# Kernel tuning notes

Hardware: AMD Instinct MI355X
Metric: run time of the kernel (lower is better)

Reference implementation:

```python
import jax, jax.numpy as jnp
import numpy as np

VOCAB = 1024
PRED_H = 320
ENC_H = 1024
JOINT_H = 640


def setup_inputs() -> dict:
    key = jax.random.key(0)
    k_f, k_g, k_w1, k_b1, k_w2, k_b2 = jax.random.split(key, 6)
    B, T, U = 8, 256, 65
    f = jax.random.normal(k_f, (B, T, ENC_H), dtype=jnp.float32)
    g = jax.random.normal(k_g, (B, U, PRED_H), dtype=jnp.float32)
    in_dim = PRED_H + ENC_H
    s1 = 1.0 / np.sqrt(in_dim)
    s2 = 1.0 / np.sqrt(JOINT_H)
    # W1 acts on cat([f, g], axis=-1): rows [0:ENC_H] hit f, rows [ENC_H:] hit g
    W1 = jax.random.uniform(k_w1, (in_dim, JOINT_H), minval=-s1, maxval=s1, dtype=jnp.float32)
    b1 = jax.random.uniform(k_b1, (JOINT_H,), minval=-s1, maxval=s1, dtype=jnp.float32)
    W2 = jax.random.uniform(k_w2, (JOINT_H, VOCAB), minval=-s2, maxval=s2, dtype=jnp.float32)
    b2 = jax.random.uniform(k_b2, (VOCAB,), minval=-s2, maxval=s2, dtype=jnp.float32)
    return {"f": f, "g": g, "W1": W1, "b1": b1, "W2": W2, "b2": b2}


def reference(f, g, W1, b1, W2, b2):
    # Linear(cat(f_expand, g_expand)) == f @ W1[:ENC_H] + g @ W1[ENC_H:] + b1,
    # broadcast-added over (T, U). Same math as the torch module (dropout p=0 / eval).
    W1f = W1[:ENC_H]          # (ENC_H, JOINT_H)
    W1g = W1[ENC_H:]          # (PRED_H, JOINT_H)
    hf = jnp.einsum("bth,hj->btj", f, W1f)            # (B, T, J)
    hg = jnp.einsum("buh,hj->buj", g, W1g)            # (B, U, J)
    h = jax.nn.relu(hf[:, :, None, :] + hg[:, None, :, :] + b1)  # (B, T, U, J)
    logits = jnp.einsum("btuj,jk->btuk", h, W2) + b2  # (B, T, U, VOCAB)
    return logits
```

## Files before the change

kernel.cpp:

```cpp
#include <hip/hip_runtime.h>
#include <cstdint>

typedef __bf16 bf16;
typedef __bf16 bf16x8 __attribute__((ext_vector_type(8)));
typedef float  f32x4  __attribute__((ext_vector_type(4)));

#define BARRIER()    asm volatile("s_barrier" ::: "memory")
#define WAIT_LGKM0() asm volatile("s_waitcnt lgkmcnt(0)" ::: "memory")
#define WAIT_VM(n)   asm volatile("s_waitcnt vmcnt(" #n ")" ::: "memory")

__device__ void gemm_small_body(
    const float* __restrict__ A, const float* __restrict__ Bm,
    const float* __restrict__ bias, bf16* __restrict__ Cout,
    int M, int N, int K, int bx, int by)
{
    __shared__ float As[64][20];
    __shared__ float Bs[16][68];
    const int tid = threadIdx.x;
    const int m0 = bx * 64, n0 = by * 64;
    const int tx = tid & 15, ty = tid >> 4;
    const int arow = tid >> 2, ak = (tid & 3) << 2;
    const int bk = tid >> 4, bc = (tid & 15) << 2;
    const bool avalid = (m0 + arow) < M;
    float acc[4][4] = {};

    for (int k0 = 0; k0 < K; k0 += 16) {
        float4 av = make_float4(0.f, 0.f, 0.f, 0.f);
        if (avalid) av = *(const float4*)&A[(size_t)(m0 + arow) * K + k0 + ak];
        float4 bv = *(const float4*)&Bm[(size_t)(k0 + bk) * N + n0 + bc];
        __syncthreads();
        *(float4*)&As[arow][ak] = av;
        *(float4*)&Bs[bk][bc] = bv;
        __syncthreads();
#pragma unroll
        for (int k = 0; k < 16; ++k) {
            float a[4], b[4];
#pragma unroll
            for (int i = 0; i < 4; ++i) a[i] = As[ty * 4 + i][k];
#pragma unroll
            for (int j = 0; j < 4; ++j) b[j] = Bs[k][tx * 4 + j];
#pragma unroll
            for (int i = 0; i < 4; ++i)
#pragma unroll
                for (int j = 0; j < 4; ++j) acc[i][j] += a[i] * b[j];
        }
    }
#pragma unroll
    for (int i = 0; i < 4; ++i) {
        int row = m0 + ty * 4 + i;
        if (row >= M) continue;
#pragma unroll
        for (int j = 0; j < 4; ++j) {
            int col = n0 + tx * 4 + j;
            float v = acc[i][j] + (bias ? bias[col] : 0.f);
            Cout[(size_t)row * N + col] = (bf16)v;
        }
    }
}

__device__ void w2t_body(const float* __restrict__ W2, bf16* __restrict__ W2T,
                         int bx, int by)
{
    __shared__ float t[32][33];
    const int tx = threadIdx.x & 31, ty = threadIdx.x >> 5;
    const int n0 = bx * 32, k0 = by * 32;
#pragma unroll
    for (int i = 0; i < 4; ++i)
        t[ty + i * 8][tx] = W2[(size_t)(k0 + ty + i * 8) * 1024 + n0 + tx];
    __syncthreads();
#pragma unroll
    for (int i = 0; i < 4; ++i)
        W2T[(size_t)(n0 + ty + i * 8) * 640 + k0 + tx] = (bf16)t[tx][ty + i * 8];
}

__global__ __launch_bounds__(256) void prep(
    const float* __restrict__ f, const float* __restrict__ g,
    const float* __restrict__ W1, const float* __restrict__ b1,
    const float* __restrict__ W2,
    bf16* __restrict__ hf, bf16* __restrict__ hgb, bf16* __restrict__ W2T)
{
    const int bid = blockIdx.x;
    if (bid < 320) {
        gemm_small_body(f, W1, nullptr, hf, 2048, 640, 1024, bid % 32, bid / 32);
    } else if (bid < 410) {
        int b = bid - 320;
        gemm_small_body(g, W1 + 1024 * 640, b1, hgb, 520, 640, 320, b % 9, b / 9);
    } else {
        int b = bid - 410;
        w2t_body(W2, W2T, b % 32, b / 32);
    }
}

__global__ __launch_bounds__(256, 3) void joint_main(
    const bf16* __restrict__ hf, const bf16* __restrict__ hgb,
    const bf16* __restrict__ W2T, const float* __restrict__ b2,
    float* __restrict__ out)
{
    __shared__ bf16 As[128 * 64];
    __shared__ bf16 Bs[2][128 * 64];
    const int tid = threadIdx.x;
    const int n0 = blockIdx.x * 128;
    const int m0 = blockIdx.y * 128;

    const int r  = tid >> 1;
    const int kh = (tid & 1) << 5;
    const int c0 = (tid & 1) << 2;
    int aoff[4];
#pragma unroll
    for (int c = 0; c < 4; ++c)
        aoff[c] = r * 64 + (((c0 + c) ^ (r & 7)) << 3);

    const int m  = m0 + r;
    const int bt = m / 65;
    const int uu = m - bt * 65;
    const int bb = bt >> 8;
    const bf16* hfp = hf  + (size_t)bt * 640 + kh;
    const bf16* hgp = hgb + (size_t)(bb * 65 + uu) * 640 + kh;

    const int wid = tid >> 6, lane = tid & 63;
    const int wr = wid >> 1, wc = wid & 1;
    const int lg = lane >> 4, l15 = lane & 15;

    f32x4 acc[4][4] = {};
    bf16x8 F[4], G[4];

    auto loadA = [&](int k0) {
#pragma unroll
        for (int i = 0; i < 4; ++i) {
            F[i] = *(const bf16x8*)(hfp + k0 + i * 8);
            G[i] = *(const bf16x8*)(hgp + k0 + i * 8);
        }
    };
    auto stageB = [&](int buf, int k0) {
        const char* w2b = (const char*)W2T + (size_t)k0 * 2;
#pragma unroll
        for (int call = 0; call < 4; ++call) {
            int chunk = call * 256 + tid;
            int brow = chunk >> 3, c = chunk & 7;
            const char* src = w2b + (size_t)(n0 + brow) * 1280
                                  + ((c ^ (brow & 7)) << 4);
            __builtin_amdgcn_global_load_lds(
                (const __attribute__((address_space(1))) uint32_t*)src,
                (__attribute__((address_space(3))) uint32_t*)&Bs[buf][chunk << 3],
                16, 0, 0);
        }
    };
    auto genA = [&]() {
#pragma unroll
        for (int c = 0; c < 4; ++c) {
            bf16x8 O;
#pragma unroll
            for (int i = 0; i < 8; ++i) {
                float s = (float)F[c][i] + (float)G[c][i];
                O[i] = (bf16)fmaxf(s, 0.f);
            }
            *(bf16x8*)&As[aoff[c]] = O;
        }
    };
    auto mfmaPhase = [&](int buf) {
        __builtin_amdgcn_s_setprio(1);
#pragma unroll
        for (int kk = 0; kk < 2; ++kk) {
            const int clog = (kk << 2) + lg;
            bf16x8 bfr[4], afr[4];
#pragma unroll
            for (int ni = 0; ni < 4; ++ni) {
                int row = wc * 64 + ni * 16 + l15;
                bfr[ni] = *(const bf16x8*)&Bs[buf][row * 64 + ((clog ^ (row & 7)) << 3)];
            }
#pragma unroll
            for (int mi = 0; mi < 4; ++mi) {
                int row = wr * 64 + mi * 16 + l15;
                afr[mi] = *(const bf16x8*)&As[row * 64 + ((clog ^ (row & 7)) << 3)];
            }
#pragma unroll
            for (int mi = 0; mi < 4; ++mi)
#pragma unroll
                for (int ni = 0; ni < 4; ++ni)
                    acc[mi][ni] = __builtin_amdgcn_mfma_f32_16x16x32_bf16(
                        afr[mi], bfr[ni], acc[mi][ni], 0, 0, 0);
        }
        __builtin_amdgcn_s_setprio(0);
    };

    loadA(0);
    stageB(0, 0);

#pragma unroll 1
    for (int t = 0; t < 10; ++t) {
        const int bufB = t & 1;
        genA();
        if (t < 9) {
            loadA((t + 1) * 64);
            stageB(bufB ^ 1, (t + 1) * 64);
            WAIT_VM(12);
        } else {
            WAIT_VM(0);
        }
        WAIT_LGKM0();
        BARRIER();
        mfmaPhase(bufB);
        BARRIER();
    }

    float bv[4];
#pragma unroll
    for (int ni = 0; ni < 4; ++ni) bv[ni] = b2[n0 + wc * 64 + ni * 16 + l15];
#pragma unroll
    for (int mi = 0; mi < 4; ++mi) {
#pragma unroll
        for (int ni = 0; ni < 4; ++ni) {
            int col = n0 + wc * 64 + ni * 16 + l15;
#pragma unroll
            for (int j = 0; j < 4; ++j) {
                int row = m0 + wr * 64 + mi * 16 + lg * 4 + j;
                out[(size_t)row * 1024 + col] = acc[mi][ni][j] + bv[ni];
            }
        }
    }
}

extern "C" void kernel_launch(void* const* d_in, const int* in_sizes, int n_in,
                              void* d_out, int out_size, void* d_ws, size_t ws_size,
                              hipStream_t stream)
{
    const float* f  = (const float*)d_in[0];
    const float* g  = (const float*)d_in[1];
    const float* W1 = (const float*)d_in[2];
    const float* b1 = (const float*)d_in[3];
    const float* W2 = (const float*)d_in[4];
    const float* b2 = (const float*)d_in[5];
    float* out = (float*)d_out;

    bf16* hf  = (bf16*)d_ws;
    bf16* hgb = hf + 2048 * 640;
    bf16* W2T = hgb + 520 * 640;

    prep<<<1050, 256, 0, stream>>>(f, g, W1, b1, W2, hf, hgb, W2T);
    joint_main<<<dim3(8, 1040), 256, 0, stream>>>(hf, hgb, W2T, b2, out);
}
```

Measured before the change: 331.9 us.

## Build MFMA A fragments directly in registers instead of staging through LDS

Removes the A tile from shared memory: each lane loads the hf and hg rows for its MFMA A fragments straight from global memory and applies the add plus ReLU in registers. The k-step is split into two half-phases so the fragment loads for the next half overlap the MFMAs of the current one, and one barrier and all LDS traffic for A go away. In exchange, the two waves that share the same rows each load and convert that A data, doubling those global reads (likely L1/L2 hits) and the VALU conversion work.

Result: slower. 664.6 us (+100.2%).

```diff
diff --git a/kernel.cpp b/kernel.cpp
--- a/kernel.cpp
+++ b/kernel.cpp
@@ -96,39 +96,48 @@
     const bf16* __restrict__ W2T, const float* __restrict__ b2,
     float* __restrict__ out)
 {
-    __shared__ bf16 As[128 * 64];
     __shared__ bf16 Bs[2][128 * 64];
     const int tid = threadIdx.x;
     const int n0 = blockIdx.x * 128;
     const int m0 = blockIdx.y * 128;
 
-    const int r  = tid >> 1;
-    const int kh = (tid & 1) << 5;
-    const int c0 = (tid & 1) << 2;
-    int aoff[4];
-#pragma unroll
-    for (int c = 0; c < 4; ++c)
-        aoff[c] = r * 64 + (((c0 + c) ^ (r & 7)) << 3);
-
-    const int m  = m0 + r;
-    const int bt = m / 65;
-    const int uu = m - bt * 65;
-    const int bb = bt >> 8;
-    const bf16* hfp = hf  + (size_t)bt * 640 + kh;
-    const bf16* hgp = hgb + (size_t)(bb * 65 + uu) * 640 + kh;
-
     const int wid = tid >> 6, lane = tid & 63;
     const int wr = wid >> 1, wc = wid & 1;
     const int lg = lane >> 4, l15 = lane & 15;
 
+    const bf16* hfp[4];
+    const bf16* hgp[4];
+#pragma unroll
+    for (int mi = 0; mi < 4; ++mi) {
+        int row = m0 + wr * 64 + mi * 16 + l15;
+        int bt = row / 65;
+        int uu = row - bt * 65;
+        int bb = bt >> 8;
+        hfp[mi] = hf  + (size_t)bt * 640 + lg * 8;
+        hgp[mi] = hgb + (size_t)(bb * 65 + uu) * 640 + lg * 8;
+    }
+
     f32x4 acc[4][4] = {};
-    bf16x8 F[4], G[4];
-
-    auto loadA = [&](int k0) {
-#pragma unroll
-        for (int i = 0; i < 4; ++i) {
-            F[i] = *(const bf16x8*)(hfp + k0 + i * 8);
-            G[i] = *(const bf16x8*)(hgp + k0 + i * 8);
+    bf16x8 Sf[4], Sg[4];
+    bf16x8 afr[4], bfr[4];
+
+    auto loadS = [&](int kabs) {
+#pragma unroll
+        for (int mi = 0; mi < 4; ++mi) {
+            Sf[mi] = *(const bf16x8*)(hfp[mi] + kabs);
+            Sg[mi] = *(const bf16x8*)(hgp[mi] + kabs);
+        }
+    };
+    auto genAfr = [&]() {
+#pragma unroll
+        for (int mi = 0; mi < 4; ++mi) {
+            bf16x8 O;
+#pragma unroll
+            for (int j = 0; j < 8; ++j) {
+                float s = (float)Sf[mi][j] + (float)Sg[mi][j];
+                O[j] = (bf16)fmaxf(s, 0.f);
+            }
+            afr[mi] = O;
         }
     };
     auto stageB = [&](int buf, int k0) {
@@ -145,62 +154,43 @@
                 16, 0, 0);
         }
     };
-    auto genA = [&]() {
-#pragma unroll
-        for (int c = 0; c < 4; ++c) {
-            bf16x8 O;
-#pragma unroll
-            for (int i = 0; i < 8; ++i) {
-                float s = (float)F[c][i] + (float)G[c][i];
-                O[i] = (bf16)fmaxf(s, 0.f);
-            }
-            *(bf16x8*)&As[aoff[c]] = O;
-        }
-    };
-    auto mfmaPhase = [&](int buf) {
+    auto mfmaHalf = [&](int buf, int kk) {
+        const int clog = (kk << 2) + lg;
+#pragma unroll
+        for (int ni = 0; ni < 4; ++ni) {
+            int row = wc * 64 + ni * 16 + l15;
+            bfr[ni] = *(const bf16x8*)&Bs[buf][row * 64 + ((clog ^ (row & 7)) << 3)];
+        }
         __builtin_amdgcn_s_setprio(1);
 #pragma unroll
-        for (int kk = 0; kk < 2; ++kk) {
-            const int clog = (kk << 2) + lg;
-            bf16x8 bfr[4], afr[4];
-#pragma unroll
-            for (int ni = 0; ni < 4; ++ni) {
-                int row = wc * 64 + ni * 16 + l15;
-                bfr[ni] = *(const bf16x8*)&Bs[buf][row * 64 + ((clog ^ (row & 7)) << 3)];
-            }
-#pragma unroll
-            for (int mi = 0; mi < 4; ++mi) {
-                int row = wr * 64 + mi * 16 + l15;
-                afr[mi] = *(const bf16x8*)&As[row * 64 + ((clog ^ (row & 7)) << 3)];
-            }
-#pragma unroll
-            for (int mi = 0; mi < 4; ++mi)
-#pragma unroll
-                for (int ni = 0; ni < 4; ++ni)
-                    acc[mi][ni] = __builtin_amdgcn_mfma_f32_16x16x32_bf16(
-                        afr[mi], bfr[ni], acc[mi][ni], 0, 0, 0);
-        }
+        for (int mi = 0; mi < 4; ++mi)
+#pragma unroll
+            for (int ni = 0; ni < 4; ++ni)
+                acc[mi][ni] = __builtin_amdgcn_mfma_f32_16x16x32_bf16(
+                    afr[mi], bfr[ni], acc[mi][ni], 0, 0, 0);
         __builtin_amdgcn_s_setprio(0);
     };
 
-    loadA(0);
     stageB(0, 0);
+    loadS(0);
 
 #pragma unroll 1
     for (int t = 0; t < 10; ++t) {
-        const int bufB = t & 1;
-        genA();
+        const int cur = t & 1;
+        BARRIER();
         if (t < 9) {
-            loadA((t + 1) * 64);
-            stageB(bufB ^ 1, (t + 1) * 64);
+            stageB(cur ^ 1, (t + 1) * 64);
             WAIT_VM(12);
         } else {
-            WAIT_VM(0);
-        }
-        WAIT_LGKM0();
+            WAIT_VM(8);
+        }
         BARRIER();
-        mfmaPhase(bufB);
-        BARRIER();
+        genAfr();
+        loadS(t * 64 + 32);
+        mfmaHalf(cur, 0);
+        genAfr();
+        if (t < 9) loadS((t + 1) * 64);
+        mfmaHalf(cur, 1);
     }
 
     float bv[4];
```

## Widen joint GEMM tile to 128x256 and interleave A generation with MFMA phases

Applied to the files above, without the earlier changes.

The joint kernel's N tile doubles from 128 to 256. Each wave now owns a full 128-row by 64-column strip, so it holds twice as many accumulators, and launch bounds drop to two blocks per SIMD. The K loop is split into four half-phases. LDS fragment loads, the next tile's global loads and the relu(hf+hg) A-tile generation are spread across those phases, each thread group handling half the K chunks at different points. The aim is to reuse each generated A tile over more output columns and overlap A production with MFMA work. The cost is higher register pressure, lower occupancy and more barriers per k-step.

New measurement: 358.8 us. 1.08x slower.

```diff
diff --git a/kernel.cpp b/kernel.cpp
--- a/kernel.cpp
+++ b/kernel.cpp
@@ -91,50 +91,64 @@
     }
 }
 
-__global__ __launch_bounds__(256, 3) void joint_main(
+__global__ __launch_bounds__(256, 2) void joint_main(
     const bf16* __restrict__ hf, const bf16* __restrict__ hgb,
     const bf16* __restrict__ W2T, const float* __restrict__ b2,
     float* __restrict__ out)
 {
     __shared__ bf16 As[128 * 64];
-    __shared__ bf16 Bs[2][128 * 64];
+    __shared__ bf16 Bs[2][256 * 64];
     const int tid = threadIdx.x;
-    const int n0 = blockIdx.x * 128;
+    const int n0 = blockIdx.x * 256;
     const int m0 = blockIdx.y * 128;
 
-    const int r  = tid >> 1;
-    const int kh = (tid & 1) << 5;
-    const int c0 = (tid & 1) << 2;
+    const int r  = tid & 127;
+    const int kh = tid >> 7;
     int aoff[4];
 #pragma unroll
-    for (int c = 0; c < 4; ++c)
-        aoff[c] = r * 64 + (((c0 + c) ^ (r & 7)) << 3);
-
+    for (int c = 0; c < 4; ++c) {
+        int cc = kh * 4 + c;
+        aoff[c] = r * 64 + ((cc ^ (r & 7)) << 3);
+    }
     const int m  = m0 + r;
     const int bt = m / 65;
     const int uu = m - bt * 65;
     const int bb = bt >> 8;
-    const bf16* hfp = hf  + (size_t)bt * 640 + kh;
-    const bf16* hgp = hgb + (size_t)(bb * 65 + uu) * 640 + kh;
+    const bf16* hfp = hf  + (size_t)bt * 640 + kh * 32;
+    const bf16* hgp = hgb + (size_t)(bb * 65 + uu) * 640 + kh * 32;
+    const bool genrole1 = (kh == 1);
 
     const int wid = tid >> 6, lane = tid & 63;
-    const int wr = wid >> 1, wc = wid & 1;
+    const int wc = wid;
     const int lg = lane >> 4, l15 = lane & 15;
 
-    f32x4 acc[4][4] = {};
-    bf16x8 F[4], G[4];
+    f32x4 acc[8][4] = {};
+    bf16x8 SF[4], SG[4];
+    bf16x8 afr[4], bfr[4];
 
     auto loadA = [&](int k0) {
 #pragma unroll
-        for (int i = 0; i < 4; ++i) {
-            F[i] = *(const bf16x8*)(hfp + k0 + i * 8);
-            G[i] = *(const bf16x8*)(hgp + k0 + i * 8);
+        for (int c = 0; c < 4; ++c) {
+            SF[c] = *(const bf16x8*)(hfp + k0 + c * 8);
+            SG[c] = *(const bf16x8*)(hgp + k0 + c * 8);
+        }
+    };
+    auto genA = [&]() {
+#pragma unroll
+        for (int c = 0; c < 4; ++c) {
+            bf16x8 O;
+#pragma unroll
+            for (int i = 0; i < 8; ++i) {
+                float s = (float)SF[c][i] + (float)SG[c][i];
+                O[i] = (bf16)fmaxf(s, 0.f);
+            }
+            *(bf16x8*)&As[aoff[c]] = O;
         }
     };
     auto stageB = [&](int buf, int k0) {
         const char* w2b = (const char*)W2T + (size_t)k0 * 2;
 #pragma unroll
-        for (int call = 0; call < 4; ++call) {
+        for (int call = 0; call < 8; ++call) {
             int chunk = call * 256 + tid;
             int brow = chunk >> 3, c = chunk & 7;
             const char* src = w2b + (size_t)(n0 + brow) * 1280
@@ -145,61 +159,60 @@
                 16, 0, 0);
         }
     };
-    auto genA = [&]() {
-#pragma unroll
-        for (int c = 0; c < 4; ++c) {
-            bf16x8 O;
-#pragma unroll
-            for (int i = 0; i < 8; ++i) {
-                float s = (float)F[c][i] + (float)G[c][i];
-                O[i] = (bf16)fmaxf(s, 0.f);
-            }
-            *(bf16x8*)&As[aoff[c]] = O;
-        }
-    };
-    auto mfmaPhase = [&](int buf) {
+    auto LDB = [&](int buf, int kk) {
+#pragma unroll
+        for (int ni = 0; ni < 4; ++ni) {
+            int row = wc * 64 + ni * 16 + l15;
+            bfr[ni] = *(const bf16x8*)&Bs[buf][row * 64 + ((((kk << 2) + lg) ^ (row & 7)) << 3)];
+        }
+    };
+    auto LDA = [&](int kk, int mh) {
+#pragma unroll
+        for (int i = 0; i < 4; ++i) {
+            int row = (mh * 4 + i) * 16 + l15;
+            afr[i] = *(const bf16x8*)&As[row * 64 + ((((kk << 2) + lg) ^ (row & 7)) << 3)];
+        }
+    };
+    auto MFMA16 = [&](int mh) {
         __builtin_amdgcn_s_setprio(1);
 #pragma unroll
-        for (int kk = 0; kk < 2; ++kk) {
-            const int clog = (kk << 2) + lg;
-            bf16x8 bfr[4], afr[4];
-#pragma unroll
-            for (int ni = 0; ni < 4; ++ni) {
-                int row = wc * 64 + ni * 16 + l15;
-                bfr[ni] = *(const bf16x8*)&Bs[buf][row * 64 + ((clog ^ (row & 7)) << 3)];
-            }
-#pragma unroll
-            for (int mi = 0; mi < 4; ++mi) {
-                int row = wr * 64 + mi * 16 + l15;
-                afr[mi] = *(const bf16x8*)&As[row * 64 + ((clog ^ (row & 7)) << 3)];
-            }
-#pragma unroll
-            for (int mi = 0; mi < 4; ++mi)
-#pragma unroll
-                for (int ni = 0; ni < 4; ++ni)
-                    acc[mi][ni] = __builtin_amdgcn_mfma_f32_16x16x32_bf16(
-                        afr[mi], bfr[ni], acc[mi][ni], 0, 0, 0);
-        }
+        for (int i = 0; i < 4; ++i)
+#pragma unroll
+            for (int ni = 0; ni < 4; ++ni)
+                acc[mh * 4 + i][ni] = __builtin_amdgcn_mfma_f32_16x16x32_bf16(
+                    afr[i], bfr[ni], acc[mh * 4 + i][ni], 0, 0, 0);
         __builtin_amdgcn_s_setprio(0);
     };
 
+    stageB(0, 0);
     loadA(0);
-    stageB(0, 0);
+    genA();
+    WAIT_LGKM0();
+    BARRIER();
 
 #pragma unroll 1
     for (int t = 0; t < 10; ++t) {
-        const int bufB = t & 1;
-        genA();
-        if (t < 9) {
-            loadA((t + 1) * 64);
-            stageB(bufB ^ 1, (t + 1) * 64);
-            WAIT_VM(12);
-        } else {
-            WAIT_VM(0);
-        }
-        WAIT_LGKM0();
-        BARRIER();
-        mfmaPhase(bufB);
+        const int cur = t & 1, nxt = cur ^ 1;
+        if (t > 0 && genrole1) genA();
+        if (t < 9) stageB(nxt, (t + 1) * 64);
+        LDB(cur, 0); LDA(0, 0);
+        BARRIER(); WAIT_LGKM0();
+        MFMA16(0);
+        BARRIER();
+        if (t < 9) loadA((t + 1) * 64);
+        LDA(0, 1);
+        BARRIER(); WAIT_LGKM0();
+        MFMA16(1);
+        BARRIER();
+        LDB(cur, 1); LDA(1, 0);
+        BARRIER(); WAIT_LGKM0();
+        MFMA16(0);
+        BARRIER();
+        if (t < 9 && !genrole1) genA();
+        LDA(1, 1);
+        if (t < 9) WAIT_VM(8);
+        BARRIER(); WAIT_LGKM0();
+        MFMA16(1);
         BARRIER();
     }
 
@@ -207,13 +220,13 @@
 #pragma unroll
     for (int ni = 0; ni < 4; ++ni) bv[ni] = b2[n0 + wc * 64 + ni * 16 + l15];
 #pragma unroll
-    for (int mi = 0; mi < 4; ++mi) {
+    for (int mi = 0; mi < 8; ++mi) {
 #pragma unroll
         for (int ni = 0; ni < 4; ++ni) {
             int col = n0 + wc * 64 + ni * 16 + l15;
 #pragma unroll
             for (int j = 0; j < 4; ++j) {
-                int row = m0 + wr * 64 + mi * 16 + lg * 4 + j;
+                int row = m0 + mi * 16 + lg * 4 + j;
                 out[(size_t)row * 1024 + col] = acc[mi][ni][j] + bv[ni];
             }
         }
@@ -237,5 +250,5 @@
     bf16* W2T = hgb + 520 * 640;
 
     prep<<<1050, 256, 0, stream>>>(f, g, W1, b1, W2, hf, hgb, W2T);
-    joint_main<<<dim3(8, 1040), 256, 0, stream>>>(hf, hgb, W2T, b2, out);
-}
+    joint_main<<<dim3(4, 1040), 256, 0, stream>>>(hf, hgb, W2T, b2, out);
+}
```
